# Kernel optimization log

Hardware: AMD Instinct MI355X
Metric: run time of the kernel (lower is better)

Reference implementation:

```python
import jax, jax.numpy as jnp
import numpy as np

B, L, D = 2, 2048, 2048
H, G, HS = 32, 8, 64  # n_heads, n_query_groups, head_size
NEG = -1e30


def setup_inputs() -> dict:
    key = jax.random.key(0)
    ks = jax.random.split(key, 7)
    s = 1.0 / np.sqrt(D)
    return {
        "x": jax.random.normal(ks[0], (B, L, D), jnp.float32),
        "cos": jax.random.uniform(ks[1], (L, HS), jnp.float32),
        "sin": jax.random.uniform(ks[2], (L, HS), jnp.float32),
        "Wq": jax.random.normal(ks[3], (D, D), jnp.float32) * s,
        "Wk": jax.random.normal(ks[4], (G * HS, D), jnp.float32) * s,
        "Wv": jax.random.normal(ks[5], (G * HS, D), jnp.float32) * s,
        "Wo": jax.random.normal(ks[6], (D, D), jnp.float32) * s,
    }


def _apply_rope(t, cos, sin):
    # t: (B, h, L, HS); cos/sin: (L, HS) broadcast over (B, h)
    x1, x2 = t[..., : HS // 2], t[..., HS // 2 :]
    rotated = jnp.concatenate((-x2, x1), axis=-1)
    return (t * cos + rotated * sin).astype(t.dtype)


def reference(x, cos, sin, Wq, Wk, Wv, Wo):
    # projections (torch Linear: y = x @ W.T)
    q = jnp.einsum("bld,ed->ble", x, Wq).reshape(B, L, H, HS).transpose(0, 2, 1, 3)
    k = jnp.einsum("bld,ed->ble", x, Wk).reshape(B, L, G, HS).transpose(0, 2, 1, 3)
    v = jnp.einsum("bld,ed->ble", x, Wv).reshape(B, L, G, HS).transpose(0, 2, 1, 3)
    q = _apply_rope(q, cos, sin)
    k = _apply_rope(k, cos, sin)
    # GQA expand: each group repeated H//G consecutive times (matches expand+reshape)
    k = jnp.repeat(k, H // G, axis=1)
    v = jnp.repeat(v, H // G, axis=1)
    scale = 1.0 / np.sqrt(HS)
    scores = jnp.einsum("bhqd,bhkd->bhqk", q, k) * scale
    causal = jnp.tril(jnp.ones((L, L), bool))
    scores = jnp.where(causal, scores, NEG)
    attn = jax.nn.softmax(scores, axis=-1)
    o = jnp.einsum("bhqk,bhkd->bhqd", attn, v)  # (B,H,L,HS)
    o = o.transpose(0, 2, 1, 3).reshape(B, L, D)
    return jnp.einsum("bld,ed->ble", o, Wo)
```

## Files before the change

### kernel.cpp

```cpp
#include <hip/hip_runtime.h>

typedef __bf16 bf16;
typedef __bf16 bf16x4 __attribute__((ext_vector_type(4)));
typedef __bf16 bf16x8 __attribute__((ext_vector_type(8)));
typedef float  f32x4  __attribute__((ext_vector_type(4)));
typedef float  f32x16 __attribute__((ext_vector_type(16)));

#define GLDS16(gsrc, ldst)                                                    \
  __builtin_amdgcn_global_load_lds(                                          \
      (const __attribute__((address_space(1))) void*)(gsrc),                 \
      (__attribute__((address_space(3))) void*)(ldst), 16, 0, 0)

#define MFMA16(a, b, c) __builtin_amdgcn_mfma_f32_16x16x32_bf16((a), (b), (c), 0, 0, 0)
#define MFMA32(a, b, c) __builtin_amdgcn_mfma_f32_32x32x16_bf16((a), (b), (c), 0, 0, 0)
#define PLSWAP(a, b) asm volatile("v_permlane32_swap_b32 %0, %1" : "+v"(a), "+v"(b))

__device__ inline unsigned pk2(float a, float b) {
  union { bf16 h[2]; unsigned u; } t;
  t.h[0] = (bf16)a; t.h[1] = (bf16)b;
  return t.u;
}
__device__ inline float ex2(float x) { return __builtin_amdgcn_exp2f(x); }

__global__ __launch_bounds__(256) void cvt5_kernel(const float* __restrict__ x,
                                                   const float* __restrict__ wq,
                                                   const float* __restrict__ wk,
                                                   const float* __restrict__ wv,
                                                   const float* __restrict__ wo,
                                                   bf16* __restrict__ xb,
                                                   bf16* __restrict__ wqkv,
                                                   bf16* __restrict__ wob) {
  int i = blockIdx.x * 256 + threadIdx.x;
  const float* src; bf16* dst; int off;
  if (i < 2097152)      { src = x;  dst = xb;             off = i; }
  else if (i < 3145728) { src = wq; dst = wqkv;           off = i - 2097152; }
  else if (i < 3407872) { src = wk; dst = wqkv + 4194304; off = i - 3145728; }
  else if (i < 3670016) { src = wv; dst = wqkv + 5242880; off = i - 3407872; }
  else                  { src = wo; dst = wob;            off = i - 3670016; }
  f32x4 f = *(const f32x4*)(src + (size_t)off * 4);
  bf16x4 o4;
#pragma unroll
  for (int j = 0; j < 4; ++j) o4[j] = (bf16)f[j];
  *(bf16x4*)(dst + (size_t)off * 4) = o4;
}

__global__ __launch_bounds__(256) void vtr_kernel(const bf16* __restrict__ v,
                                                  bf16* __restrict__ vt) {
  constexpr int L = 2048, QS = 3072;
  const int kv0 = blockIdx.x * 64;
  const int bg = blockIdx.y;
  const int tid = threadIdx.x;
  __shared__ bf16 t[64 * 64];

#pragma unroll
  for (int i = 0; i < 2; ++i) {
    int c = tid + 256 * i;
    int kv = c >> 3, e = c & 7;
    bf16x8 row = *(const bf16x8*)(v + (size_t)((bg >> 3) * L + kv0 + kv) * QS +
                                  (bg & 7) * 64 + e * 8);
#pragma unroll
    for (int j = 0; j < 8; ++j)
      t[(8 * e + j) * 64 + (kv ^ (8 * (e ^ j)))] = row[j];
  }
  __syncthreads();

  const int d = tid >> 2, c4 = tid & 3;
  bf16* orow = vt + ((size_t)bg * 64 + d) * L + kv0;
#pragma unroll
  for (int dl = 0; dl < 2; ++dl) {
    int sc = 2 * c4 + dl;
    bf16x8 ch = *(const bf16x8*)&t[d * 64 + 8 * (sc ^ (d >> 3))];
    *(bf16x8*)(orow + 8 * sc) = ch;
  }
}

template <typename OutT, bool ROPE>
__global__ __launch_bounds__(256) void gemm_bt(const bf16* __restrict__ A,
                                               const bf16* __restrict__ Bm,
                                               OutT* __restrict__ C,
                                               int M, int N, int K,
                                               const float* __restrict__ cosb,
                                               const float* __restrict__ sinb) {
  __shared__ bf16 a_lds[128 * 32];
  __shared__ bf16 b_lds[128 * 32];
  const int tid = threadIdx.x;
  const int w = tid >> 6, lane = tid & 63;
  const int lr = lane & 15, lg = lane >> 4;
  const int wr = w >> 1, wc = w & 1;
  const int nbx = N >> 7;
  const int nwg = (M >> 7) * nbx;
  const int bid = blockIdx.x;
  const int sid = (bid & 7) * (nwg >> 3) + (bid >> 3);
  const int m0 = (sid / nbx) << 7, n0 = (sid % nbx) << 7;

  f32x4 acc[4][4];
#pragma unroll
  for (int i = 0; i < 4; ++i)
#pragma unroll
    for (int j = 0; j < 4; ++j) acc[i][j] = f32x4{0.f, 0.f, 0.f, 0.f};

  const int srow = tid >> 2, skc = (tid & 3) * 8;
  const bf16* ap0 = A  + (size_t)(m0 + srow) * K + skc;
  const bf16* ap1 = A  + (size_t)(m0 + srow + 64) * K + skc;
  const bf16* bp0 = Bm + (size_t)(n0 + srow) * K + skc;
  const bf16* bp1 = Bm + (size_t)(n0 + srow + 64) * K + skc;
  bf16* const lA0 = &a_lds[w * 512];
  bf16* const lA1 = &a_lds[w * 512 + 2048];
  bf16* const lB0 = &b_lds[w * 512];
  bf16* const lB1 = &b_lds[w * 512 + 2048];

  for (int kt = 0; kt < K; kt += 32) {
    GLDS16(ap0, lA0);
    GLDS16(ap1, lA1);
    GLDS16(bp0, lB0);
    GLDS16(bp1, lB1);
    ap0 += 32; ap1 += 32; bp0 += 32; bp1 += 32;
    __syncthreads();
    bf16x8 af[4], bfr[4];
#pragma unroll
    for (int t = 0; t < 4; ++t) {
      af[t]  = *(const bf16x8*)&a_lds[(wr * 64 + t * 16 + lr) * 32 + lg * 8];
      bfr[t] = *(const bf16x8*)&b_lds[(wc * 64 + t * 16 + lr) * 32 + lg * 8];
    }
#pragma unroll
    for (int mt = 0; mt < 4; ++mt)
#pragma unroll
      for (int nt = 0; nt < 4; ++nt)
        acc[mt][nt] = MFMA16(af[mt], bfr[nt], acc[mt][nt]);
    __syncthreads();
  }

  const int hb = (n0 + wc * 64) >> 6;
  const bool dorope = ROPE && (hb < 40);
  const float rsc = (ROPE && hb < 32) ? 0.18033688011112042f : 1.0f;

#pragma unroll
  for (int mt = 0; mt < 4; ++mt)
#pragma unroll
    for (int r = 0; r < 4; ++r) {
      int mm = m0 + wr * 64 + mt * 16 + 4 * lg + r;
      float ov[4];
      if (dorope) {
        int l = mm & 2047;
        const float* cp = cosb + l * 64 + lr;
        const float* sp = sinb + l * 64 + lr;
        float a0 = acc[mt][0][r], a1 = acc[mt][1][r];
        float a2 = acc[mt][2][r], a3 = acc[mt][3][r];
        ov[0] = (a0 * cp[0]  - a2 * sp[0])  * rsc;
        ov[1] = (a1 * cp[16] - a3 * sp[16]) * rsc;
        ov[2] = (a2 * cp[32] + a0 * sp[32]) * rsc;
        ov[3] = (a3 * cp[48] + a1 * sp[48]) * rsc;
      } else {
#pragma unroll
        for (int nt = 0; nt < 4; ++nt) ov[nt] = acc[mt][nt][r];
      }
#pragma unroll
      for (int nt = 0; nt < 4; ++nt) {
        int nn = n0 + wc * 64 + nt * 16 + lr;
        C[(size_t)mm * N + nn] = (OutT)ov[nt];
      }
    }
}

__global__ __launch_bounds__(256, 4) void attn_kernel(const bf16* __restrict__ q,
                                                      const bf16* __restrict__ k,
                                                      const bf16* __restrict__ vtg,
                                                      bf16* __restrict__ o,
                                                      bf16* __restrict__ opart,
                                                      float* __restrict__ mpart,
                                                      float* __restrict__ lpart,
                                                      int split_n, int umax) {
  constexpr int L = 2048;
  constexpr int QS = 3072;
  constexpr int OS = 2048;
  const int id = blockIdx.x;
  int bh, u, ts, te, pidx;
  bool split;
  if (id < split_n) {
    bh = id & 63;
    int t = id >> 6;
    u = 15 - (t >> 1);
    int s = t & 1;
    ts = s * (u + 1);
    te = ts + (u + 1);
    pidx = (bh * 9 + (u - 7)) * 2 + s;
    split = true;
  } else {
    int e = id - split_n;
    bh = e & 63;
    u = umax - (e >> 6);
    ts = 0;
    te = 2 * u + 2;
    pidx = 0;
    split = false;
  }
  const int q0 = u * 128;
  const int b = bh >> 5, h = bh & 31, g = h >> 2;
  const int tid = threadIdx.x;
  const int w = tid >> 6, lane = tid & 63;
  const int lc = lane & 31;
  const int H  = lane >> 5;
  const int off4 = 4 * H;
  const int qw = q0 + w * 32;
  const int qg = qw + lc;

  __shared__ bf16 k_lds[2][64 * 64];
  __shared__ bf16 vt_lds[2][64 * 64];

  bf16x8 qf[4];
  {
    const bf16* qrow = q + (size_t)(b * L + qg) * QS + h * 64 + 8 * H;
#pragma unroll
    for (int s = 0; s < 4; ++s) qf[s] = *(const bf16x8*)(qrow + 16 * s);
  }

  f32x16 acc0, acc1;
#pragma unroll
  for (int r = 0; r < 16; ++r) { acc0[r] = 0.f; acc1[r] = 0.f; }
  float m_run = -1e30f, l_run = 0.f;

  const bf16* vbase = vtg + (size_t)(b * 8 + g) * 64 * L;

  const int kvr = tid >> 3, c8 = tid & 7;
  const bf16* kp0 = k + (size_t)(b * L + ts * 64 + kvr) * QS + g * 64 + ((c8 ^ (kvr & 7)) * 8);
  const bf16* kp1 = kp0 + (size_t)32 * QS;
  const bf16* vp0 = vbase + (size_t)kvr * L + ts * 64 + c8 * 8;
  const bf16* vp1 = vp0 + (size_t)32 * L;

  auto stageK = [&](int buf) {
    GLDS16(kp0, &k_lds[buf][w * 512]);
    GLDS16(kp1, &k_lds[buf][w * 512 + 2048]);
    kp0 += (size_t)64 * QS; kp1 += (size_t)64 * QS;
  };
  auto stageV = [&](int buf) {
    GLDS16(vp0, &vt_lds[buf][w * 512]);
    GLDS16(vp1, &vt_lds[buf][w * 512 + 2048]);
    vp0 += 64; vp1 += 64;
  };

  stageK(0);
  stageV(0);
  __syncthreads();

  for (int it = ts; it < te; ++it) {
    const int cur = (it - ts) & 1;
    const int kv0 = it * 64;
    const bool notlast = (it + 1 < te);
    if (notlast) {
      stageK(cur ^ 1);
      stageV(cur ^ 1);
    }

    if (kv0 <= qw + 31) {
      f32x16 p0, p1;
#pragma unroll
      for (int r = 0; r < 16; ++r) { p0[r] = 0.f; p1[r] = 0.f; }
      __builtin_amdgcn_s_setprio(1);
#pragma unroll
      for (int s = 0; s < 4; ++s) {
        int ch = ((2 * s + H) ^ (lc & 7)) * 8;
        bf16x8 kf0 = *(const bf16x8*)&k_lds[cur][lc * 64 + ch];
        bf16x8 kf1 = *(const bf16x8*)&k_lds[cur][(32 + lc) * 64 + ch];
        p0 = MFMA32(kf0, qf[s], p0);
        p1 = MFMA32(kf1, qf[s], p1);
      }
      __builtin_amdgcn_s_setprio(0);

      if (kv0 + 63 > qw) {
#pragma unroll
        for (int r = 0; r < 16; ++r) {
          int kvl = kv0 + (r & 3) + 8 * (r >> 2) + off4;
          if (kvl > qg)      p0[r] = -1e30f;
          if (kvl + 32 > qg) p1[r] = -1e30f;
        }
      }

      float mt = -1e30f;
#pragma unroll
      for (int r = 0; r < 16; ++r) mt = fmaxf(mt, fmaxf(p0[r], p1[r]));
      mt = fmaxf(mt, __shfl_xor(mt, 32));
      const int defer = __all(mt <= m_run + 11.0f);
      float alpha = 1.f;
      if (!defer) {
        float mn = fmaxf(m_run, mt);
        alpha = ex2(m_run - mn);
        m_run = mn;
      }
      float ls = 0.f;
#pragma unroll
      for (int r = 0; r < 16; ++r) {
        p0[r] = ex2(p0[r] - m_run);
        p1[r] = ex2(p1[r] - m_run);
        ls += p0[r] + p1[r];
      }
      ls += __shfl_xor(ls, 32);
      l_run = l_run * alpha + ls;
      if (!defer) {
#pragma unroll
        for (int r = 0; r < 16; ++r) {
          float aq = __shfl(alpha, ((r & 3) + 8 * (r >> 2)) + off4);
          acc0[r] *= aq;
          acc1[r] *= aq;
        }
      }

      unsigned A[16];
#pragma unroll
      for (int i = 0; i < 8; ++i) {
        A[i]     = pk2(p0[2 * i], p0[2 * i + 1]);
        A[8 + i] = pk2(p1[2 * i], p1[2 * i + 1]);
      }
#pragma unroll
      for (int base = 0; base < 16; base += 4) {
        PLSWAP(A[base],     A[base + 2]);
        PLSWAP(A[base + 1], A[base + 3]);
      }

      __builtin_amdgcn_s_setprio(1);
#pragma unroll
      for (int sp = 0; sp < 4; ++sp) {
        union { unsigned u[4]; bf16x8 v8; } pa;
#pragma unroll
        for (int jx = 0; jx < 4; ++jx) pa.u[jx] = A[4 * sp + jx];
        int ch = ((2 * sp + H) ^ (lc & 7)) * 8;
        bf16x8 vf0 = *(const bf16x8*)&vt_lds[cur][lc * 64 + ch];
        bf16x8 vf1 = *(const bf16x8*)&vt_lds[cur][(32 + lc) * 64 + ch];
        acc0 = MFMA32(pa.v8, vf0, acc0);
        acc1 = MFMA32(pa.v8, vf1, acc1);
      }
      __builtin_amdgcn_s_setprio(0);
    }

    __syncthreads();
  }

  if (split) {
    bf16* op = opart + (size_t)pidx * (128 * 64);
#pragma unroll
    for (int r = 0; r < 16; ++r) {
      int qrow = w * 32 + (r & 3) + 8 * (r >> 2) + off4;
      op[qrow * 64 + lc]      = (bf16)acc0[r];
      op[qrow * 64 + 32 + lc] = (bf16)acc1[r];
    }
    if (H == 0) {
      mpart[(size_t)pidx * 128 + w * 32 + lc] = m_run;
      lpart[(size_t)pidx * 128 + w * 32 + lc] = l_run;
    }
  } else {
#pragma unroll
    for (int r = 0; r < 16; ++r) {
      int qrow = (r & 3) + 8 * (r >> 2) + off4;
      float lq = __shfl(l_run, qrow);
      float inv = 1.f / lq;
      size_t orow = (size_t)(b * L + qw + qrow) * OS + h * 64;
      o[orow + lc]      = (bf16)(acc0[r] * inv);
      o[orow + 32 + lc] = (bf16)(acc1[r] * inv);
    }
  }
}

__global__ __launch_bounds__(256) void comb_kernel(const bf16* __restrict__ opart,
                                                   const float* __restrict__ mpart,
                                                   const float* __restrict__ lpart,
                                                   bf16* __restrict__ o) {
  constexpr int L = 2048, OS = 2048;
  const int blk = blockIdx.x;
  const int bh = blk / 9, uu = blk % 9, u = uu + 7;
  const int b = bh >> 5, h = bh & 31;
  const int q0 = u * 128;
  const int t = threadIdx.x;
  const int row = t >> 1, dh = (t & 1) * 32;

  const size_t s0 = (size_t)blk * 2, s1 = s0 + 1;
  float m0 = mpart[s0 * 128 + row], m1 = mpart[s1 * 128 + row];
  float l0 = lpart[s0 * 128 + row], l1 = lpart[s1 * 128 + row];
  float m = fmaxf(m0, m1);
  float w0 = ex2(m0 - m), w1 = ex2(m1 - m);
  float inv = 1.f / (l0 * w0 + l1 * w1);

  const bf16* O0 = opart + s0 * (128 * 64) + row * 64 + dh;
  const bf16* O1 = opart + s1 * (128 * 64) + row * 64 + dh;
  bf16* orow = o + (size_t)(b * L + q0 + row) * OS + h * 64 + dh;
#pragma unroll
  for (int j = 0; j < 4; ++j) {
    bf16x8 a = *(const bf16x8*)(O0 + 8 * j);
    bf16x8 c = *(const bf16x8*)(O1 + 8 * j);
    bf16x8 r;
#pragma unroll
    for (int e = 0; e < 8; ++e)
      r[e] = (bf16)(((float)a[e] * w0 + (float)c[e] * w1) * inv);
    *(bf16x8*)(orow + 8 * j) = r;
  }
}

extern "C" void kernel_launch(void* const* d_in, const int* in_sizes, int n_in,
                              void* d_out, int out_size, void* d_ws, size_t ws_size,
                              hipStream_t stream) {
  (void)in_sizes; (void)n_in; (void)out_size;
  const float* x    = (const float*)d_in[0];
  const float* cosb = (const float*)d_in[1];
  const float* sinb = (const float*)d_in[2];
  const float* Wq   = (const float*)d_in[3];
  const float* Wk   = (const float*)d_in[4];
  const float* Wv   = (const float*)d_in[5];
  const float* Wo   = (const float*)d_in[6];

  constexpr int B = 2, L = 2048, D = 2048, H = 32, G = 8;
  constexpr int M = B * L;
  constexpr int DKV = G * 64;
  constexpr int NQKV = D + 2 * DKV;

  char* p = (char*)d_ws;
  bf16*  xb   = (bf16*)p;  p += (size_t)M * D * 2;
  bf16*  wqkv = (bf16*)p;  p += (size_t)NQKV * D * 2;
  bf16*  wob  = (bf16*)p;  p += (size_t)D * D * 2;
  bf16*  qkv  = (bf16*)p;  p += (size_t)M * NQKV * 2;
  bf16*  vtg  = (bf16*)p;  p += (size_t)B * G * 64 * L * 2;
  bf16*  opart = (bf16*)p; p += (size_t)1152 * 128 * 64 * 2;
  float* mpart = (float*)p; p += (size_t)1152 * 128 * 4;
  float* lpart = (float*)p; p += (size_t)1152 * 128 * 4;
  bf16*  ob   = xb;

  const bool do_split = ws_size >= (size_t)(p - (char*)d_ws);

  cvt5_kernel<<<dim3(18432), 256, 0, stream>>>(x, Wq, Wk, Wv, Wo, xb, wqkv, wob);

  gemm_bt<bf16, true><<<dim3((NQKV / 128) * (M / 128)), 256, 0, stream>>>(
      xb, wqkv, qkv, M, NQKV, D, cosb, sinb);

  vtr_kernel<<<dim3(L / 64, B * G), 256, 0, stream>>>(qkv + D + DKV, vtg);

  if (do_split) {
    attn_kernel<<<dim3(1600), 256, 0, stream>>>(qkv, qkv + D, vtg, ob,
                                                opart, mpart, lpart, 1152, 6);
    comb_kernel<<<dim3(576), 256, 0, stream>>>(opart, mpart, lpart, ob);
  } else {
    attn_kernel<<<dim3(1024), 256, 0, stream>>>(qkv, qkv + D, vtg, ob,
                                                opart, mpart, lpart, 0, 15);
  }

  gemm_bt<float, false><<<dim3((D / 128) * (M / 128)), 256, 0, stream>>>(
      ob, wob, (float*)d_out, M, D, D, nullptr, nullptr);
}
```

Baseline: 223.6 us.

## Double GEMM K-tile to 64 with XOR-swizzled LDS layout

```diff
diff --git a/kernel.cpp b/kernel.cpp
--- a/kernel.cpp
+++ b/kernel.cpp
@@ -81,8 +81,8 @@
                                                int M, int N, int K,
                                                const float* __restrict__ cosb,
                                                const float* __restrict__ sinb) {
-  __shared__ bf16 a_lds[128 * 32];
-  __shared__ bf16 b_lds[128 * 32];
+  __shared__ bf16 a_lds[128 * 64];
+  __shared__ bf16 b_lds[128 * 64];
   const int tid = threadIdx.x;
   const int w = tid >> 6, lane = tid & 63;
   const int lr = lane & 15, lg = lane >> 4;
@@ -99,34 +99,43 @@
 #pragma unroll
     for (int j = 0; j < 4; ++j) acc[i][j] = f32x4{0.f, 0.f, 0.f, 0.f};
 
-  const int srow = tid >> 2, skc = (tid & 3) * 8;
-  const bf16* ap0 = A  + (size_t)(m0 + srow) * K + skc;
-  const bf16* ap1 = A  + (size_t)(m0 + srow + 64) * K + skc;
-  const bf16* bp0 = Bm + (size_t)(n0 + srow) * K + skc;
-  const bf16* bp1 = Bm + (size_t)(n0 + srow + 64) * K + skc;
-  bf16* const lA0 = &a_lds[w * 512];
-  bf16* const lA1 = &a_lds[w * 512 + 2048];
-  bf16* const lB0 = &b_lds[w * 512];
-  bf16* const lB1 = &b_lds[w * 512 + 2048];
-
-  for (int kt = 0; kt < K; kt += 32) {
-    GLDS16(ap0, lA0);
-    GLDS16(ap1, lA1);
-    GLDS16(bp0, lB0);
-    GLDS16(bp1, lB1);
-    ap0 += 32; ap1 += 32; bp0 += 32; bp1 += 32;
+  const bf16* ap[4];
+  const bf16* bp[4];
+#pragma unroll
+  for (int i = 0; i < 4; ++i) {
+    int ci = tid + 256 * i;
+    int row = ci >> 3, c = ci & 7;
+    int cs = c ^ (row & 7);
+    ap[i] = A  + (size_t)(m0 + row) * K + cs * 8;
+    bp[i] = Bm + (size_t)(n0 + row) * K + cs * 8;
+  }
+
+  for (int kt = 0; kt < K; kt += 64) {
+#pragma unroll
+    for (int i = 0; i < 4; ++i) {
+      GLDS16(ap[i], &a_lds[w * 512 + i * 2048]);
+      GLDS16(bp[i], &b_lds[w * 512 + i * 2048]);
+      ap[i] += 64; bp[i] += 64;
+    }
     __syncthreads();
-    bf16x8 af[4], bfr[4];
+    bf16x8 af[4][2], bfr[4][2];
 #pragma unroll
     for (int t = 0; t < 4; ++t) {
-      af[t]  = *(const bf16x8*)&a_lds[(wr * 64 + t * 16 + lr) * 32 + lg * 8];
-      bfr[t] = *(const bf16x8*)&b_lds[(wc * 64 + t * 16 + lr) * 32 + lg * 8];
+      int ra = wr * 64 + t * 16 + lr;
+      int rb = wc * 64 + t * 16 + lr;
+#pragma unroll
+      for (int kc = 0; kc < 2; ++kc) {
+        af[t][kc]  = *(const bf16x8*)&a_lds[ra * 64 + (((4 * kc + lg) ^ (ra & 7)) * 8)];
+        bfr[t][kc] = *(const bf16x8*)&b_lds[rb * 64 + (((4 * kc + lg) ^ (rb & 7)) * 8)];
+      }
     }
 #pragma unroll
     for (int mt = 0; mt < 4; ++mt)
 #pragma unroll
       for (int nt = 0; nt < 4; ++nt)
-        acc[mt][nt] = MFMA16(af[mt], bfr[nt], acc[mt][nt]);
+#pragma unroll
+        for (int kc = 0; kc < 2; ++kc)
+          acc[mt][nt] = MFMA16(af[mt][kc], bfr[nt][kc], acc[mt][nt]);
     __syncthreads();
   }
 
```

After: 223.0 us. No clear change (-0.3%).
